# Kernel optimization log

Measured on AMD Instinct MI355X. Metric: run time of the kernel, lower is better.

## Reference

```python
import jax, jax.numpy as jnp
import numpy as np

NEG_SLOPE = 0.2


def gat_layer(x, src, dst, W, att_src, att_dst, bias, concat):
    # x: [N, Fin]; W: [Fin, H*C]; att_*: [H, C]; bias: [H*C] or [C]
    n = x.shape[0]
    H, C = att_src.shape
    h = (x @ W).reshape(n, H, C)                      # [N,H,C]
    a_src = jnp.einsum('nhc,hc->nh', h, att_src)      # [N,H]
    a_dst = jnp.einsum('nhc,hc->nh', h, att_dst)      # [N,H]
    e = a_src[src] + a_dst[dst]                       # [E,H]
    e = jnp.where(e > 0, e, NEG_SLOPE * e)            # leaky_relu(0.2)
    # segment softmax over edges grouped by destination node
    m = jax.ops.segment_max(e, dst, num_segments=n)   # [N,H]
    m = jnp.where(jnp.isfinite(m), m, 0.0)            # empty segments
    ex = jnp.exp(e - m[dst])                          # [E,H]
    s = jax.ops.segment_sum(ex, dst, num_segments=n)  # [N,H]
    alpha = ex / (s[dst] + 1e-16)                     # [E,H]
    msg = h[src] * alpha[..., None]                   # [E,H,C]
    out = jax.ops.segment_sum(msg, dst, num_segments=n)  # [N,H,C]
    out = out.reshape(n, H * C) if concat else out.mean(axis=1)
    return out + bias


def setup_inputs() -> dict:
    key = jax.random.key(0)
    ks = jax.random.split(key, 10)
    N, E, FIN, HID, HEADS, OUT = 50000, 800000, 128, 64, 4, 16
    x = jax.random.normal(ks[0], (N, FIN), dtype=jnp.float32)
    edge_index = jax.random.randint(ks[1], (2, E), 0, N, dtype=jnp.int32)
    sc = 0.05
    return {
        'x': x,
        'edge_index': edge_index,
        'W1': jax.random.normal(ks[2], (FIN, HEADS * HID), jnp.float32) * sc,
        'att_src1': jax.random.normal(ks[3], (HEADS, HID), jnp.float32) * sc,
        'att_dst1': jax.random.normal(ks[4], (HEADS, HID), jnp.float32) * sc,
        'b1': jnp.zeros((HEADS * HID,), jnp.float32),
        'W2': jax.random.normal(ks[5], (HEADS * HID, OUT), jnp.float32) * sc,
        'att_src2': jax.random.normal(ks[6], (1, OUT), jnp.float32) * sc,
        'att_dst2': jax.random.normal(ks[7], (1, OUT), jnp.float32) * sc,
        'b2': jnp.zeros((OUT,), jnp.float32),
    }


def reference(x, edge_index, W1, att_src1, att_dst1, b1, W2, att_src2, att_dst2, b2):
    src, dst = edge_index[0], edge_index[1]
    h = gat_layer(x, src, dst, W1, att_src1, att_dst1, b1, concat=True)
    h = jax.nn.relu(h)
    # dropout is identity in eval mode
    out = gat_layer(h, src, dst, W2, att_src2, att_dst2, b2, concat=False)
    return out
```

## Files before the change

kernel.cpp:

```cpp
#include <hip/hip_runtime.h>
#include <hip/hip_bf16.h>

#define FIN 128
#define HC 256
#define H1 4
#define C1 64
#define OUT2 16

typedef __attribute__((ext_vector_type(8))) short bf16x8;
typedef __attribute__((ext_vector_type(4))) float f32x4;

__device__ inline float bf2f(unsigned short u) {
    union { unsigned int i; float f; } v; v.i = ((unsigned int)u) << 16; return v.f;
}
__device__ inline unsigned short f2bf(float f) {
    union { float f; unsigned int i; } v; v.f = f;
    unsigned int i = v.i;
    return (unsigned short)((i + 0x7FFFu + ((i >> 16) & 1u)) >> 16);
}
__device__ inline unsigned int pack2(float a, float b) {
    return (unsigned int)f2bf(a) | ((unsigned int)f2bf(b) << 16);
}

__global__ __launch_bounds__(256) void prep_kernel(
    const float* __restrict__ W1, unsigned short* __restrict__ W1t,
    const int* __restrict__ dst, int* __restrict__ counts, int E)
{
    int b = blockIdx.x;
    if (b < 128) {
        int t = b * 256 + threadIdx.x;
        int c = t >> 7, k = t & 127;
        W1t[t] = f2bf(W1[k * HC + c]);
    } else {
        int e = (b - 128) * 256 + threadIdx.x;
        if (e < E) atomicAdd(&counts[dst[e]], 1);
    }
}

__global__ __launch_bounds__(256) void gemm1_mfma_kernel(
    const float* __restrict__ x, const unsigned short* __restrict__ W1t,
    const float* __restrict__ att_src, const float* __restrict__ att_dst,
    unsigned short* __restrict__ h1, float* __restrict__ a_src,
    float* __restrict__ a_dst, int N)
{
    const int t  = threadIdx.x;
    const int wv = t >> 6;
    const int l  = t & 63;
    const int c0 = l & 15;
    const int h  = l >> 4;
    const int R0 = blockIdx.x * 64 + wv * 16;

    f32x4 acc[16];
    #pragma unroll
    for (int j = 0; j < 16; j++) acc[j] = (f32x4){0.f, 0.f, 0.f, 0.f};

    int arow = R0 + c0;
    if (arow > N - 1) arow = N - 1;
    const float* xrow = x + (size_t)arow * FIN;

    for (int kb = 0; kb < FIN; kb += 32) {
        float4 f0 = *(const float4*)&xrow[kb + 8 * h];
        float4 f1 = *(const float4*)&xrow[kb + 8 * h + 4];
        union { bf16x8 v; unsigned int u[4]; } af;
        af.u[0] = pack2(f0.x, f0.y);
        af.u[1] = pack2(f0.z, f0.w);
        af.u[2] = pack2(f1.x, f1.y);
        af.u[3] = pack2(f1.z, f1.w);
        #pragma unroll
        for (int j = 0; j < 16; j++) {
            int col = 16 * j + c0;
            union { bf16x8 v; uint4 u; } bf;
            bf.u = *(const uint4*)&W1t[(size_t)col * FIN + kb + 8 * h];
            acc[j] = __builtin_amdgcn_mfma_f32_16x16x32_bf16(af.v, bf.v, acc[j], 0, 0, 0);
        }
    }

    float avs[16], avd[16];
    #pragma unroll
    for (int j = 0; j < 16; j++) {
        avs[j] = att_src[16 * j + c0];
        avd[j] = att_dst[16 * j + c0];
    }
    f32x4 ps[4], pd[4];
    #pragma unroll
    for (int hd = 0; hd < 4; hd++) {
        ps[hd] = (f32x4){0.f, 0.f, 0.f, 0.f};
        pd[hd] = (f32x4){0.f, 0.f, 0.f, 0.f};
        #pragma unroll
        for (int jj = 0; jj < 4; jj++) {
            int j = 4 * hd + jj;
            #pragma unroll
            for (int r = 0; r < 4; r++) {
                ps[hd][r] = fmaf(acc[j][r], avs[j], ps[hd][r]);
                pd[hd][r] = fmaf(acc[j][r], avd[j], pd[hd][r]);
            }
        }
    }
    #pragma unroll
    for (int hd = 0; hd < 4; hd++)
        #pragma unroll
        for (int r = 0; r < 4; r++) {
            float s = ps[hd][r], d = pd[hd][r];
            s += __shfl_xor(s, 1, 64);  d += __shfl_xor(d, 1, 64);
            s += __shfl_xor(s, 2, 64);  d += __shfl_xor(d, 2, 64);
            s += __shfl_xor(s, 4, 64);  d += __shfl_xor(d, 4, 64);
            s += __shfl_xor(s, 8, 64);  d += __shfl_xor(d, 8, 64);
            ps[hd][r] = s;  pd[hd][r] = d;
        }
    {
        float s_sel = 0.f, d_sel = 0.f;
        #pragma unroll
        for (int hd = 0; hd < 4; hd++)
            #pragma unroll
            for (int r = 0; r < 4; r++) {
                bool m = (c0 == hd * 4 + r);
                s_sel = m ? ps[hd][r] : s_sel;
                d_sel = m ? pd[hd][r] : d_sel;
            }
        int row = R0 + 4 * h + (c0 & 3);
        if (row < N) {
            a_src[row * 4 + (c0 >> 2)] = s_sel;
            a_dst[row * 4 + (c0 >> 2)] = d_sel;
        }
    }

    #pragma unroll
    for (int r = 0; r < 4; r++) {
        int row = R0 + 4 * h + r;
        if (row < N) {
            unsigned short* hp = &h1[(size_t)row * HC + c0];
            #pragma unroll
            for (int j = 0; j < 16; j++)
                hp[16 * j] = f2bf(acc[j][r]);
        }
    }
}

__global__ __launch_bounds__(1024) void scan1_kernel(
    const int* __restrict__ counts, int* __restrict__ rowptr,
    int* __restrict__ bsum, int n)
{
    __shared__ int sm[1024];
    int tid = threadIdx.x;
    int i = blockIdx.x * 1024 + tid;
    int v = (i < n) ? counts[i] : 0;
    sm[tid] = v;
    __syncthreads();
    for (int off = 1; off < 1024; off <<= 1) {
        int tv = (tid >= off) ? sm[tid - off] : 0;
        __syncthreads();
        sm[tid] += tv;
        __syncthreads();
    }
    if (i < n) rowptr[i] = sm[tid] - v;
    if (tid == 1023) bsum[blockIdx.x] = sm[1023];
}

__global__ __launch_bounds__(1024) void scan2_kernel(
    int* __restrict__ bsum, int* __restrict__ rowptr, int nb, int N, int E)
{
    __shared__ int sm[1024];
    int tid = threadIdx.x;
    int v = (tid < nb) ? bsum[tid] : 0;
    sm[tid] = v;
    __syncthreads();
    for (int off = 1; off < 1024; off <<= 1) {
        int tv = (tid >= off) ? sm[tid - off] : 0;
        __syncthreads();
        sm[tid] += tv;
        __syncthreads();
    }
    if (tid < nb) bsum[tid] = sm[tid] - v;
    if (tid == 0) rowptr[N] = E;
}

__global__ __launch_bounds__(1024) void scan3_kernel(
    int* __restrict__ rowptr, const int* __restrict__ bsum, int n)
{
    int i = blockIdx.x * 1024 + threadIdx.x;
    if (i < n) rowptr[i] += bsum[blockIdx.x];
}

__global__ __launch_bounds__(256) void scatter_kernel(
    const int* __restrict__ src, const int* __restrict__ dst,
    const int* __restrict__ rowptr, int* __restrict__ cursor,
    const float* __restrict__ a_src, const float* __restrict__ a_dst,
    uint4* __restrict__ csr_rec, int E)
{
    int e = blockIdx.x * blockDim.x + threadIdx.x;
    if (e >= E) return;
    int s = src[e], d = dst[e];
    int pos = rowptr[d] + atomicAdd(&cursor[d], 1);
    float4 av = *(const float4*)&a_src[(size_t)s * 4];
    float4 bv = *(const float4*)&a_dst[(size_t)d * 4];
    float w0, w1, w2, w3, v;
    v = av.x + bv.x; v = v > 0.f ? v : 0.2f * v; w0 = __expf(v);
    v = av.y + bv.y; v = v > 0.f ? v : 0.2f * v; w1 = __expf(v);
    v = av.z + bv.z; v = v > 0.f ? v : 0.2f * v; w2 = __expf(v);
    v = av.w + bv.w; v = v > 0.f ? v : 0.2f * v; w3 = __expf(v);
    uint4 rec;
    rec.x = (unsigned int)s;
    rec.y = (unsigned int)d;
    rec.z = pack2(w0, w1);
    rec.w = pack2(w2, w3);
    csr_rec[pos] = rec;
}

__global__ __launch_bounds__(256) void agg1_kernel(
    const unsigned short* __restrict__ h1,
    const uint4* __restrict__ csr_rec, const int* __restrict__ rowptr,
    const float* __restrict__ b1, const float* __restrict__ W2,
    const float* __restrict__ att_src2, const float* __restrict__ att_dst2,
    float* __restrict__ h2, float* __restrict__ a_src2, float* __restrict__ a_dst2,
    int N)
{
    __shared__ float o_sh[4][256];
    int wave = (int)((blockIdx.x * blockDim.x + threadIdx.x) >> 6);
    if (wave >= N) return;
    int node = __builtin_amdgcn_readfirstlane(wave);
    int wv = (threadIdx.x >> 6);
    int l = threadIdx.x & 63;
    int h = l >> 4;
    int rs = rowptr[node], re = rowptr[node + 1];
    float a0 = 0.f, a1 = 0.f, a2 = 0.f, a3 = 0.f, sw = 0.f;
    int p = rs;
    for (; p + 8 <= re; p += 8) {
        uint4 r[8];
        #pragma unroll
        for (int j = 0; j < 8; j++) r[j] = csr_rec[p + j];
        uint2 hv[8];
        #pragma unroll
        for (int j = 0; j < 8; j++)
            hv[j] = *(const uint2*)&h1[(size_t)(int)r[j].x * HC + 4 * l];
        #pragma unroll
        for (int j = 0; j < 8; j++) {
            unsigned int wsel = (h & 2) ? r[j].w : r[j].z;
            float wv_ = bf2f((unsigned short)((h & 1) ? (wsel >> 16) : (wsel & 0xffff)));
            a0 = fmaf(wv_, bf2f((unsigned short)(hv[j].x & 0xffff)), a0);
            a1 = fmaf(wv_, bf2f((unsigned short)(hv[j].x >> 16)), a1);
            a2 = fmaf(wv_, bf2f((unsigned short)(hv[j].y & 0xffff)), a2);
            a3 = fmaf(wv_, bf2f((unsigned short)(hv[j].y >> 16)), a3);
            sw += wv_;
        }
    }
    for (; p < re; p++) {
        uint4 r = csr_rec[p];
        uint2 hv = *(const uint2*)&h1[(size_t)(int)r.x * HC + 4 * l];
        unsigned int wsel = (h & 2) ? r.w : r.z;
        float wv_ = bf2f((unsigned short)((h & 1) ? (wsel >> 16) : (wsel & 0xffff)));
        a0 = fmaf(wv_, bf2f((unsigned short)(hv.x & 0xffff)), a0);
        a1 = fmaf(wv_, bf2f((unsigned short)(hv.x >> 16)), a1);
        a2 = fmaf(wv_, bf2f((unsigned short)(hv.y & 0xffff)), a2);
        a3 = fmaf(wv_, bf2f((unsigned short)(hv.y >> 16)), a3);
        sw += wv_;
    }
    float inv = 1.f / (sw + 1e-16f);
    float4 bv = *(const float4*)&b1[4 * l];
    float o0 = fmaxf(a0 * inv + bv.x, 0.f);
    float o1 = fmaxf(a1 * inv + bv.y, 0.f);
    float o2 = fmaxf(a2 * inv + bv.z, 0.f);
    float o3 = fmaxf(a3 * inv + bv.w, 0.f);

    float* my = o_sh[wv];
    *(float4*)&my[4 * l] = make_float4(o0, o1, o2, o3);
    asm volatile("s_waitcnt lgkmcnt(0)" ::: "memory");
    __builtin_amdgcn_sched_barrier(0);
    float part = 0.f;
    int q = h;
    #pragma unroll
    for (int j = 0; j < 64; j++)
        part = fmaf(my[q + 4 * j], W2[64 * j + l], part);
    part += __shfl_xor(part, 16, 64);
    part += __shfl_xor(part, 32, 64);
    int c = l & 15;
    float ps = part * att_src2[c];
    float pdv = part * att_dst2[c];
    ps += __shfl_xor(ps, 1, 64);  pdv += __shfl_xor(pdv, 1, 64);
    ps += __shfl_xor(ps, 2, 64);  pdv += __shfl_xor(pdv, 2, 64);
    ps += __shfl_xor(ps, 4, 64);  pdv += __shfl_xor(pdv, 4, 64);
    ps += __shfl_xor(ps, 8, 64);  pdv += __shfl_xor(pdv, 8, 64);
    if (l == 0) { a_src2[node] = ps; a_dst2[node] = pdv; }
    if (l < 16) h2[(size_t)node * OUT2 + l] = part;
}

__global__ __launch_bounds__(256) void agg2_kernel(
    const float* __restrict__ h2,
    const int* __restrict__ csr_rec_i,
    const float* __restrict__ a_src2, const float* __restrict__ a_dst2,
    const int* __restrict__ rowptr,
    const float* __restrict__ b2, float* __restrict__ out, int N)
{
    int wave = (int)((blockIdx.x * blockDim.x + threadIdx.x) >> 6);
    if (wave >= N) return;
    int node = __builtin_amdgcn_readfirstlane(wave);
    int l = threadIdx.x & 63;
    int g = l >> 4, c = l & 15;
    int rs = rowptr[node], re = rowptr[node + 1];
    float ad = a_dst2[node];
    float acc = 0.f, sw = 0.f;
    int p = rs + g;
    for (; p + 4 < re; p += 8) {
        int sn0 = csr_rec_i[(size_t)p * 4];
        int sn1 = csr_rec_i[(size_t)(p + 4) * 4];
        float e0 = a_src2[sn0] + ad;
        float e1 = a_src2[sn1] + ad;
        float x0 = h2[(size_t)sn0 * OUT2 + c];
        float x1 = h2[(size_t)sn1 * OUT2 + c];
        e0 = e0 > 0.f ? e0 : 0.2f * e0;
        e1 = e1 > 0.f ? e1 : 0.2f * e1;
        float w0 = __expf(e0);
        float w1 = __expf(e1);
        acc = fmaf(w0, x0, acc);
        acc = fmaf(w1, x1, acc);
        sw += w0 + w1;
    }
    if (p < re) {
        int sn = csr_rec_i[(size_t)p * 4];
        float e0 = a_src2[sn] + ad;
        e0 = e0 > 0.f ? e0 : 0.2f * e0;
        float w0 = __expf(e0);
        acc = fmaf(w0, h2[(size_t)sn * OUT2 + c], acc);
        sw += w0;
    }
    acc += __shfl_xor(acc, 16, 64);
    acc += __shfl_xor(acc, 32, 64);
    sw += __shfl_xor(sw, 16, 64);
    sw += __shfl_xor(sw, 32, 64);
    if (l < 16)
        out[(size_t)node * OUT2 + l] = acc / (sw + 1e-16f) + b2[l];
}

extern "C" void kernel_launch(void* const* d_in, const int* in_sizes, int n_in,
                              void* d_out, int out_size, void* d_ws, size_t ws_size,
                              hipStream_t stream)
{
    const float* x        = (const float*)d_in[0];
    const int*   ei       = (const int*)d_in[1];
    const float* W1       = (const float*)d_in[2];
    const float* att_src1 = (const float*)d_in[3];
    const float* att_dst1 = (const float*)d_in[4];
    const float* b1       = (const float*)d_in[5];
    const float* W2       = (const float*)d_in[6];
    const float* att_src2 = (const float*)d_in[7];
    const float* att_dst2 = (const float*)d_in[8];
    const float* b2       = (const float*)d_in[9];
    float* out = (float*)d_out;

    const int N = in_sizes[0] / FIN;
    const int E = in_sizes[1] / 2;
    const int* srcv = ei;
    const int* dstv = ei + E;

    char* base = (char*)d_ws;
    #define ALLOC(ptr, type, nelem) \
        type* ptr = (type*)base; base += (((size_t)(nelem) * sizeof(type) + 255) & ~(size_t)255);
    ALLOC(h1,      unsigned short, (size_t)N * HC)
    ALLOC(csr_rec, uint4,          (size_t)E)
    ALLOC(h2,      float,          (size_t)N * OUT2)
    ALLOC(a_src1v, float,          (size_t)N * 4)
    ALLOC(a_dst1v, float,          (size_t)N * 4)
    ALLOC(a_src2v, float,          (size_t)N)
    ALLOC(a_dst2v, float,          (size_t)N)
    ALLOC(counts,  int,            (size_t)2 * N)
    ALLOC(rowptr,  int,            (size_t)N + 1)
    ALLOC(bsum,    int,            1024)
    #undef ALLOC
    int* cursor = counts + N;
    unsigned short* W1t = (unsigned short*)csr_rec;

    const int nb = (N + 1023) / 1024;

    (void)hipMemsetAsync(counts, 0, sizeof(int) * 2 * (size_t)N, stream);

    prep_kernel<<<128 + (E + 255) / 256, 256, 0, stream>>>(W1, W1t, dstv, counts, E);
    gemm1_mfma_kernel<<<(N + 63) / 64, 256, 0, stream>>>(x, W1t, att_src1, att_dst1,
                                                         h1, a_src1v, a_dst1v, N);
    scan1_kernel<<<nb, 1024, 0, stream>>>(counts, rowptr, bsum, N);
    scan2_kernel<<<1, 1024, 0, stream>>>(bsum, rowptr, nb, N, E);
    scan3_kernel<<<nb, 1024, 0, stream>>>(rowptr, bsum, N);
    scatter_kernel<<<(E + 255) / 256, 256, 0, stream>>>(srcv, dstv, rowptr, cursor,
                                                        a_src1v, a_dst1v, csr_rec, E);
    agg1_kernel<<<(N + 3) / 4, 256, 0, stream>>>(h1, csr_rec, rowptr, b1, W2,
                                                 att_src2, att_dst2,
                                                 h2, a_src2v, a_dst2v, N);
    agg2_kernel<<<(N + 3) / 4, 256, 0, stream>>>(h2, (const int*)csr_rec,
                                                 a_src2v, a_dst2v, rowptr, b2, out, N);
}
```

Baseline: 221.0 us.

## Drop scan3 pass by folding block offsets into consumers; rework agg1 W2 matvec and agg2 unroll

Removes the third scan kernel by having scatter, agg1 and agg2 add the per-block prefix from bsum when reading rowptr, and compute the last row end from E. In agg1, the hidden-to-output matvec now reads float4 chunks from a padded shared buffer with per-head contiguous layout and indexes W2 by head. agg2 unrolls the edge loop to four edges per lane group to raise memory-level parallelism. This saves one launch and one pass over rowptr, at the cost of extra bsum loads in three kernels and more registers in agg2.

```diff
diff --git a/kernel.cpp b/kernel.cpp
--- a/kernel.cpp
+++ b/kernel.cpp
@@ -157,7 +157,7 @@
 }
 
 __global__ __launch_bounds__(1024) void scan2_kernel(
-    int* __restrict__ bsum, int* __restrict__ rowptr, int nb, int N, int E)
+    int* __restrict__ bsum, int nb)
 {
     __shared__ int sm[1024];
     int tid = threadIdx.x;
@@ -171,26 +171,19 @@
         __syncthreads();
     }
     if (tid < nb) bsum[tid] = sm[tid] - v;
-    if (tid == 0) rowptr[N] = E;
-}
-
-__global__ __launch_bounds__(1024) void scan3_kernel(
-    int* __restrict__ rowptr, const int* __restrict__ bsum, int n)
-{
-    int i = blockIdx.x * 1024 + threadIdx.x;
-    if (i < n) rowptr[i] += bsum[blockIdx.x];
 }
 
 __global__ __launch_bounds__(256) void scatter_kernel(
     const int* __restrict__ src, const int* __restrict__ dst,
-    const int* __restrict__ rowptr, int* __restrict__ cursor,
+    const int* __restrict__ rowptr, const int* __restrict__ bsum,
+    int* __restrict__ cursor,
     const float* __restrict__ a_src, const float* __restrict__ a_dst,
     uint4* __restrict__ csr_rec, int E)
 {
     int e = blockIdx.x * blockDim.x + threadIdx.x;
     if (e >= E) return;
     int s = src[e], d = dst[e];
-    int pos = rowptr[d] + atomicAdd(&cursor[d], 1);
+    int pos = rowptr[d] + bsum[d >> 10] + atomicAdd(&cursor[d], 1);
     float4 av = *(const float4*)&a_src[(size_t)s * 4];
     float4 bv = *(const float4*)&a_dst[(size_t)d * 4];
     float w0, w1, w2, w3, v;
@@ -209,19 +202,21 @@
 __global__ __launch_bounds__(256) void agg1_kernel(
     const unsigned short* __restrict__ h1,
     const uint4* __restrict__ csr_rec, const int* __restrict__ rowptr,
+    const int* __restrict__ bsum,
     const float* __restrict__ b1, const float* __restrict__ W2,
     const float* __restrict__ att_src2, const float* __restrict__ att_dst2,
     float* __restrict__ h2, float* __restrict__ a_src2, float* __restrict__ a_dst2,
-    int N)
-{
-    __shared__ float o_sh[4][256];
+    int N, int E)
+{
+    __shared__ float o_sh[4][272];
     int wave = (int)((blockIdx.x * blockDim.x + threadIdx.x) >> 6);
     if (wave >= N) return;
     int node = __builtin_amdgcn_readfirstlane(wave);
     int wv = (threadIdx.x >> 6);
     int l = threadIdx.x & 63;
     int h = l >> 4;
-    int rs = rowptr[node], re = rowptr[node + 1];
+    int rs = rowptr[node] + bsum[node >> 10];
+    int re = (node + 1 == N) ? E : rowptr[node + 1] + bsum[(node + 1) >> 10];
     float a0 = 0.f, a1 = 0.f, a2 = 0.f, a3 = 0.f, sw = 0.f;
     int p = rs;
     for (; p + 8 <= re; p += 8) {
@@ -262,17 +257,23 @@
     float o3 = fmaxf(a3 * inv + bv.w, 0.f);
 
     float* my = o_sh[wv];
-    *(float4*)&my[4 * l] = make_float4(o0, o1, o2, o3);
+    *(float4*)&my[4 * l + 4 * h] = make_float4(o0, o1, o2, o3);
     asm volatile("s_waitcnt lgkmcnt(0)" ::: "memory");
     __builtin_amdgcn_sched_barrier(0);
+    int q = h;
+    int c = l & 15;
     float part = 0.f;
-    int q = h;
-    #pragma unroll
-    for (int j = 0; j < 64; j++)
-        part = fmaf(my[q + 4 * j], W2[64 * j + l], part);
+    #pragma unroll
+    for (int m = 0; m < 16; m++) {
+        float4 ov = *(const float4*)&my[68 * q + 4 * m];
+        const float* w = &W2[(size_t)(64 * q + 4 * m) * OUT2 + c];
+        part = fmaf(ov.x, w[0],  part);
+        part = fmaf(ov.y, w[16], part);
+        part = fmaf(ov.z, w[32], part);
+        part = fmaf(ov.w, w[48], part);
+    }
     part += __shfl_xor(part, 16, 64);
     part += __shfl_xor(part, 32, 64);
-    int c = l & 15;
     float ps = part * att_src2[c];
     float pdv = part * att_dst2[c];
     ps += __shfl_xor(ps, 1, 64);  pdv += __shfl_xor(pdv, 1, 64);
@@ -287,34 +288,44 @@
     const float* __restrict__ h2,
     const int* __restrict__ csr_rec_i,
     const float* __restrict__ a_src2, const float* __restrict__ a_dst2,
-    const int* __restrict__ rowptr,
-    const float* __restrict__ b2, float* __restrict__ out, int N)
+    const int* __restrict__ rowptr, const int* __restrict__ bsum,
+    const float* __restrict__ b2, float* __restrict__ out, int N, int E)
 {
     int wave = (int)((blockIdx.x * blockDim.x + threadIdx.x) >> 6);
     if (wave >= N) return;
     int node = __builtin_amdgcn_readfirstlane(wave);
     int l = threadIdx.x & 63;
     int g = l >> 4, c = l & 15;
-    int rs = rowptr[node], re = rowptr[node + 1];
+    int rs = rowptr[node] + bsum[node >> 10];
+    int re = (node + 1 == N) ? E : rowptr[node + 1] + bsum[(node + 1) >> 10];
     float ad = a_dst2[node];
     float acc = 0.f, sw = 0.f;
     int p = rs + g;
-    for (; p + 4 < re; p += 8) {
-        int sn0 = csr_rec_i[(size_t)p * 4];
-        int sn1 = csr_rec_i[(size_t)(p + 4) * 4];
+    for (; p + 12 < re; p += 16) {
+        int sn0 = csr_rec_i[(size_t)(p     ) * 4];
+        int sn1 = csr_rec_i[(size_t)(p +  4) * 4];
+        int sn2 = csr_rec_i[(size_t)(p +  8) * 4];
+        int sn3 = csr_rec_i[(size_t)(p + 12) * 4];
         float e0 = a_src2[sn0] + ad;
         float e1 = a_src2[sn1] + ad;
+        float e2 = a_src2[sn2] + ad;
+        float e3 = a_src2[sn3] + ad;
         float x0 = h2[(size_t)sn0 * OUT2 + c];
         float x1 = h2[(size_t)sn1 * OUT2 + c];
+        float x2 = h2[(size_t)sn2 * OUT2 + c];
+        float x3 = h2[(size_t)sn3 * OUT2 + c];
         e0 = e0 > 0.f ? e0 : 0.2f * e0;
         e1 = e1 > 0.f ? e1 : 0.2f * e1;
-        float w0 = __expf(e0);
-        float w1 = __expf(e1);
+        e2 = e2 > 0.f ? e2 : 0.2f * e2;
+        e3 = e3 > 0.f ? e3 : 0.2f * e3;
+        float w0 = __expf(e0), w1 = __expf(e1), w2 = __expf(e2), w3 = __expf(e3);
         acc = fmaf(w0, x0, acc);
         acc = fmaf(w1, x1, acc);
-        sw += w0 + w1;
-    }
-    if (p < re) {
+        acc = fmaf(w2, x2, acc);
+        acc = fmaf(w3, x3, acc);
+        sw += (w0 + w1) + (w2 + w3);
+    }
+    for (; p < re; p += 4) {
         int sn = csr_rec_i[(size_t)p * 4];
         float e0 = a_src2[sn] + ad;
         e0 = e0 > 0.f ? e0 : 0.2f * e0;
@@ -376,13 +387,13 @@
     gemm1_mfma_kernel<<<(N + 63) / 64, 256, 0, stream>>>(x, W1t, att_src1, att_dst1,
                                                          h1, a_src1v, a_dst1v, N);
     scan1_kernel<<<nb, 1024, 0, stream>>>(counts, rowptr, bsum, N);
-    scan2_kernel<<<1, 1024, 0, stream>>>(bsum, rowptr, nb, N, E);
-    scan3_kernel<<<nb, 1024, 0, stream>>>(rowptr, bsum, N);
-    scatter_kernel<<<(E + 255) / 256, 256, 0, stream>>>(srcv, dstv, rowptr, cursor,
+    scan2_kernel<<<1, 1024, 0, stream>>>(bsum, nb);
+    scatter_kernel<<<(E + 255) / 256, 256, 0, stream>>>(srcv, dstv, rowptr, bsum, cursor,
                                                         a_src1v, a_dst1v, csr_rec, E);
-    agg1_kernel<<<(N + 3) / 4, 256, 0, stream>>>(h1, csr_rec, rowptr, b1, W2,
+    agg1_kernel<<<(N + 3) / 4, 256, 0, stream>>>(h1, csr_rec, rowptr, bsum, b1, W2,
                                                  att_src2, att_dst2,
-                                                 h2, a_src2v, a_dst2v, N);
+                                                 h2, a_src2v, a_dst2v, N, E);
     agg2_kernel<<<(N + 3) / 4, 256, 0, stream>>>(h2, (const int*)csr_rec,
-                                                 a_src2v, a_dst2v, rowptr, b2, out, N);
-}
+                                                 a_src2v, a_dst2v, rowptr, bsum,
+                                                 b2, out, N, E);
+}
```

Result: no change. 221.4 us (+0.2%).
